# Optimization experiments

Measured on AMD Instinct MI355X. Metric: run time of the kernel, lower is better.

## Reference

```python
import jax, jax.numpy as jnp
import numpy as np

NUM_HEADS = 16
FIELD_SIZE = 512
SIGMA = 3.0
EMB = 1024


def _causal_kernel_fft(G, sigma):
    # kernel[i] = exp(-|i - G//2| / sigma) for i < G//2, else 0; normalized
    i = np.arange(G)
    dist = np.abs(i - G // 2)
    kernel = np.where(i >= G // 2, 0.0, np.exp(-dist / sigma)).astype(np.float32)
    kernel = kernel / (kernel.sum() + 1e-8)
    return jnp.asarray(np.fft.rfft(kernel), dtype=jnp.complex64)


def setup_inputs() -> dict:
    key = jax.random.key(0)
    ks = jax.random.split(key, 9)
    B, N, D = 4, 4096, EMB
    s = 1.0 / np.sqrt(D)
    return {
        "x": jax.random.normal(ks[0], (B, N, D), dtype=jnp.float32),
        "q_w": jax.random.uniform(ks[1], (D, D), minval=-s, maxval=s, dtype=jnp.float32),
        "q_b": jnp.zeros((D,), jnp.float32),
        "k_w": jax.random.uniform(ks[2], (D, D), minval=-s, maxval=s, dtype=jnp.float32),
        "k_b": jnp.zeros((D,), jnp.float32),
        "v_w": jax.random.uniform(ks[3], (D, D), minval=-s, maxval=s, dtype=jnp.float32),
        "v_b": jnp.zeros((D,), jnp.float32),
        "out_w": jax.random.uniform(ks[4], (D, D), minval=-s, maxval=s, dtype=jnp.float32),
        "out_b": jnp.zeros((D,), jnp.float32),
    }


def reference(x, q_w, q_b, k_w, k_b, v_w, v_b, out_w, out_b):
    B, N, D = x.shape
    H, hd, G = NUM_HEADS, D // NUM_HEADS, FIELD_SIZE

    # projections (q is computed in the original but unused downstream)
    q = x @ q_w.T + q_b  # noqa: F841 (faithful to original)
    k = (x @ k_w.T + k_b).reshape(B, N, H, hd).transpose(0, 2, 1, 3)  # (B,H,N,hd)
    v = (x @ v_w.T + v_b).reshape(B, N, H, hd).transpose(0, 2, 1, 3)

    # map sequence positions -> field bins (same for all b, h)
    pos = jnp.arange(N, dtype=jnp.float32) / max(N - 1, 1) * (G - 1)
    field_idx = jnp.clip(pos.astype(jnp.int32), 0, G - 1)  # (N,)

    # weighted values by key magnitude
    k_mag = jnp.linalg.norm(k, axis=-1, keepdims=True)  # (B,H,N,1)
    wv = v * k_mag  # (B,H,N,hd)

    # scatter-add tokens into field bins (vectorized over B,H,hd)
    field = jax.ops.segment_sum(wv.transpose(2, 0, 1, 3), field_idx,
                                num_segments=G)  # (G,B,H,hd)
    field = field.transpose(1, 2, 0, 3)  # (B,H,G,hd)

    # causal convolution along the field via FFT (circular, as in original)
    kfft = _causal_kernel_fft(G, SIGMA)
    f_fft = jnp.fft.rfft(field, n=G, axis=2)
    conv = jnp.fft.irfft(f_fft * kfft[None, None, :, None], n=G, axis=2)

    # gather back to token positions
    out = conv[:, :, field_idx, :]  # (B,H,N,hd)
    out = out.transpose(0, 2, 1, 3).reshape(B, N, D)
    return out @ out_w.T + out_b
```

## Files before the change

### kernel.cpp

```cpp
#include <hip/hip_runtime.h>
#include <hip/hip_bf16.h>

#define NPOS 4096
#define DIM  1024
#define GSZ  512

#define GAS __attribute__((address_space(1)))
#define LAS __attribute__((address_space(3)))

typedef __attribute__((ext_vector_type(8))) short bf16x8;
typedef __attribute__((ext_vector_type(4))) float f32x4;

__device__ __forceinline__ void async_load16(const void* g, void* l) {
  __builtin_amdgcn_global_load_lds((const GAS void*)g, (LAS void*)l, 16, 0, 0);
}

__device__ __forceinline__ int fidx_of(int n) {
  return (int)(((float)n / 4095.0f) * 511.0f);
}

__device__ __forceinline__ float bf2f(unsigned short s) {
  union { unsigned u; float f; } v; v.u = ((unsigned)s) << 16; return v.f;
}

__device__ __forceinline__ int bin_start(int g) {
  if (g >= GSZ) return NPOS;
  int i0 = (g * 4095 + 510) / 511;
  while (i0 > 0 && fidx_of(i0 - 1) >= g) --i0;
  while (i0 < NPOS && fidx_of(i0) < g) ++i0;
  return i0;
}

__device__ __forceinline__ void bin_range(int g, int& i0, int& i1) {
  i0 = bin_start(g);
  i1 = bin_start(g + 1);
}

__global__ __launch_bounds__(256) void cast_all(
    const float* __restrict__ x, const float* __restrict__ kw,
    const float* __restrict__ vw, const float* __restrict__ ow,
    __hip_bfloat16* __restrict__ xb, __hip_bfloat16* __restrict__ kvwb,
    __hip_bfloat16* __restrict__ outwb) {
  int blk = blockIdx.x;
  const float* src; __hip_bfloat16* dst; int off;
  if (blk < 8192)      { src = x;  dst = xb;              off = blk; }
  else if (blk < 8704) { src = kw; dst = kvwb;            off = blk - 8192; }
  else if (blk < 9216) { src = vw; dst = kvwb + 1048576;  off = blk - 8704; }
  else                 { src = ow; dst = outwb;           off = blk - 9216; }
  int i = (off * 256 + threadIdx.x) * 8;
  float4 f0 = *(const float4*)(src + i);
  float4 f1 = *(const float4*)(src + i + 4);
  ushort4 o0, o1;
  __hip_bfloat16 t;
  t = __float2bfloat16(f0.x); o0.x = *(unsigned short*)&t;
  t = __float2bfloat16(f0.y); o0.y = *(unsigned short*)&t;
  t = __float2bfloat16(f0.z); o0.z = *(unsigned short*)&t;
  t = __float2bfloat16(f0.w); o0.w = *(unsigned short*)&t;
  t = __float2bfloat16(f1.x); o1.x = *(unsigned short*)&t;
  t = __float2bfloat16(f1.y); o1.y = *(unsigned short*)&t;
  t = __float2bfloat16(f1.z); o1.z = *(unsigned short*)&t;
  t = __float2bfloat16(f1.w); o1.w = *(unsigned short*)&t;
  *(ushort4*)(dst + i) = o0;
  *(ushort4*)(dst + i + 4) = o1;
}


#define BAR()   __builtin_amdgcn_s_barrier()
#define LGKM0() do { asm volatile("s_waitcnt lgkmcnt(0)" ::: "memory"); \
                     __builtin_amdgcn_sched_barrier(0); } while (0)
#define VMW(N)  asm volatile("s_waitcnt vmcnt(" #N ")" ::: "memory")

#define STAGE_A(BUF, KT, C) \
  async_load16(ag0 + (size_t)(KT) * 64 + (size_t)(C) * 65536, &As[BUF][(C) * 4096 + ldst])
#define STAGE_B(BUF, KT, C) \
  async_load16(bg0 + (size_t)(KT) * 64 + (size_t)(C) * 65536, &Bs[BUF][(C) * 4096 + ldst])

#define STAGE_FULL(BUF, KT) do { \
    _Pragma("unroll") \
    for (int c_ = 0; c_ < 4; ++c_) { \
      STAGE_A(BUF, KT, c_); \
      STAGE_B(BUF, KT, c_); \
    } \
  } while (0)

#define LDA(BUF, MT, CB) (*(const bf16x8*)&As[BUF][abase + (MT) * 1024 + (CB)])
#define LDB(BUF, NT, CB) (*(const bf16x8*)&Bs[BUF][bbase + (NT) * 1024 + (CB)])

#define MFMA_Q(MQ, NQ, BF) do { \
    __builtin_amdgcn_s_setprio(1); \
    _Pragma("unroll") \
    for (int m_ = 0; m_ < 4; ++m_) { \
      _Pragma("unroll") \
      for (int n_ = 0; n_ < 2; ++n_) { \
        acc[(MQ)*4+m_][(NQ)*2+n_] = __builtin_amdgcn_mfma_f32_16x16x32_bf16( \
            af[m_][0], BF[n_][0], acc[(MQ)*4+m_][(NQ)*2+n_], 0, 0, 0); \
        acc[(MQ)*4+m_][(NQ)*2+n_] = __builtin_amdgcn_mfma_f32_16x16x32_bf16( \
            af[m_][1], BF[n_][1], acc[(MQ)*4+m_][(NQ)*2+n_], 0, 0, 0); \
      } \
    } \
    __builtin_amdgcn_s_setprio(0); \
  } while (0)

#define DO_TILE(BUF, KT) do { \
    const bool pf_ = (KT) + 2 < 16; \
     \
    _Pragma("unroll") \
    for (int m_ = 0; m_ < 4; ++m_) { af[m_][0] = LDA(BUF, m_, cb0); af[m_][1] = LDA(BUF, m_, cb1); } \
    _Pragma("unroll") \
    for (int n_ = 0; n_ < 2; ++n_) { b0f[n_][0] = LDB(BUF, n_, cb0); b0f[n_][1] = LDB(BUF, n_, cb1); } \
    BAR(); LGKM0(); \
    MFMA_Q(0, 0, b0f); \
    BAR(); \
     \
    _Pragma("unroll") \
    for (int n_ = 0; n_ < 2; ++n_) { b1f[n_][0] = LDB(BUF, 2 + n_, cb0); b1f[n_][1] = LDB(BUF, 2 + n_, cb1); } \
    if (pf_) { STAGE_A(BUF, (KT) + 2, 0); STAGE_A(BUF, (KT) + 2, 2); } \
    BAR(); LGKM0(); \
    MFMA_Q(0, 1, b1f); \
    BAR(); \
     \
    _Pragma("unroll") \
    for (int m_ = 0; m_ < 4; ++m_) { af[m_][0] = LDA(BUF, 4 + m_, cb0); af[m_][1] = LDA(BUF, 4 + m_, cb1); } \
    if (pf_) { STAGE_B(BUF, (KT) + 2, 0); STAGE_B(BUF, (KT) + 2, 1); \
               STAGE_B(BUF, (KT) + 2, 2); STAGE_B(BUF, (KT) + 2, 3); } \
    BAR(); LGKM0(); \
    MFMA_Q(1, 1, b1f); \
    BAR(); \
     \
    if (pf_) { STAGE_A(BUF, (KT) + 2, 1); STAGE_A(BUF, (KT) + 2, 3); } \
    MFMA_Q(1, 0, b0f); \
    if (pf_) { VMW(8); } else if ((KT) == 14) { VMW(0); } \
    BAR(); \
  } while (0)

__global__ __launch_bounds__(512, 2) void gemm_kv(
    const __hip_bfloat16* __restrict__ A,
    const __hip_bfloat16* __restrict__ B,
    const float* __restrict__ k_b, const float* __restrict__ v_b,
    __hip_bfloat16* __restrict__ Vb, float* __restrict__ knorm) {
  __shared__ __align__(16) __hip_bfloat16 As[2][16384];
  __shared__ __align__(16) __hip_bfloat16 Bs[2][16384];
  const int tid = threadIdx.x;

  const int l   = blockIdx.y * 64 + blockIdx.x;
  const int xcd = l & 7, j = l >> 3;
  const int bx  = xcd * 8 + (j & 7), by = j >> 3;
  const int bm  = bx * 256;

  const int sb  = ((((tid & 7) * 16) ^ (((tid >> 3) & 7) << 4)) >> 1);
  const int r0  = tid >> 3;
  const __hip_bfloat16* ag0 = A + (size_t)(bm + r0) * 1024 + sb;
  const __hip_bfloat16* bg0 = B + (size_t)(by * 256 + r0) * 1024 + sb;
  const int ldst = tid * 8;

  const int wave = tid >> 6, lane = tid & 63;
  const int wr = wave >> 2, wc = wave & 3;
  const int m16 = lane & 15, quad = lane >> 4;
  const int swz  = (m16 & 7) << 4;
  const int cb0  = ((quad * 16)      ^ swz) >> 1;
  const int cb1  = ((quad * 16 + 64) ^ swz) >> 1;
  const int abase = wr * 8192 + m16 * 64;
  const int bbase = wc * 4096 + m16 * 64;

  f32x4 acc[8][4];
#pragma unroll
  for (int i = 0; i < 8; i++)
#pragma unroll
    for (int j2 = 0; j2 < 4; j2++) acc[i][j2] = (f32x4)0.f;

  bf16x8 af[4][2], b0f[2][2], b1f[2][2];

  STAGE_FULL(0, 0);
  STAGE_FULL(1, 1);
  VMW(8);
  BAR();

  for (int kt = 0; kt < 16; kt += 2) {
    DO_TILE(0, kt);
    DO_TILE(1, kt + 1);
  }

  if (by < 4) {
    const int head = by * 4 + wc;
    float bv[4];
#pragma unroll
    for (int nt = 0; nt < 4; nt++) bv[nt] = k_b[by * 256 + wc * 64 + nt * 16 + m16];
#pragma unroll
    for (int mt = 0; mt < 8; mt++) {
#pragma unroll
      for (int r = 0; r < 4; r++) {
        float s = 0.f;
#pragma unroll
        for (int nt = 0; nt < 4; nt++) {
          float t = acc[mt][nt][r] + bv[nt];
          s += t * t;
        }
        s += __shfl_xor(s, 1);
        s += __shfl_xor(s, 2);
        s += __shfl_xor(s, 4);
        s += __shfl_xor(s, 8);
        if (m16 == 0) {
          int row = bm + wr * 128 + mt * 16 + quad * 4 + r;
          knorm[(size_t)row * 16 + head] = sqrtf(s);
        }
      }
    }
  } else {
    const int colb = (by - 4) * 256 + wc * 64;
#pragma unroll
    for (int mt = 0; mt < 8; mt++) {
#pragma unroll
      for (int nt = 0; nt < 4; nt++) {
        int col = colb + nt * 16 + m16;
        float bvv = v_b[col];
#pragma unroll
        for (int r = 0; r < 4; r++) {
          int row = bm + wr * 128 + mt * 16 + quad * 4 + r;
          Vb[(size_t)row * 1024 + col] = __float2bfloat16(acc[mt][nt][r] + bvv);
        }
      }
    }
  }
}

__global__ __launch_bounds__(256) void gemm_outc(
    const __hip_bfloat16* __restrict__ A,
    const __hip_bfloat16* __restrict__ B,
    const float* __restrict__ bias,
    float* __restrict__ C) {
  const int K = 1024;
  __shared__ __align__(16) __hip_bfloat16 Aso[64 * 32];
  __shared__ __align__(16) __hip_bfloat16 Bso[64 * 32];
  __shared__ __align__(16) float ctile[64 * 68];
  const int tid = threadIdx.x;
  const int bm = blockIdx.x * 64, bn = blockIdx.y * 64;

  const int srow = tid >> 2;
  const int scol = (tid & 3) * 8;
  const __hip_bfloat16* ap = A + (size_t)(bm + srow) * K + scol;
  const __hip_bfloat16* bp = B + (size_t)(bn + srow) * K + scol;
  __hip_bfloat16* as = &Aso[srow * 32 + scol];
  __hip_bfloat16* bs = &Bso[srow * 32 + scol];

  const int wave = tid >> 6, lane = tid & 63;
  const int wm = (wave >> 1) * 32, wn = (wave & 1) * 32;
  const int m16 = lane & 15, quad = lane >> 4;

  f32x4 acc[2][2];
#pragma unroll
  for (int i = 0; i < 2; i++)
#pragma unroll
    for (int j = 0; j < 2; j++) acc[i][j] = (f32x4)0.f;

  for (int k0 = 0; k0 < K; k0 += 32) {
    async_load16(ap + k0, as);
    async_load16(bp + k0, bs);
    __syncthreads();
    bf16x8 afr[2], bfr[2];
#pragma unroll
    for (int mt = 0; mt < 2; mt++)
      afr[mt] = *(const bf16x8*)&Aso[(wm + mt * 16 + m16) * 32 + quad * 8];
#pragma unroll
    for (int nt = 0; nt < 2; nt++)
      bfr[nt] = *(const bf16x8*)&Bso[(wn + nt * 16 + m16) * 32 + quad * 8];
#pragma unroll
    for (int mt = 0; mt < 2; mt++)
#pragma unroll
      for (int nt = 0; nt < 2; nt++)
        acc[mt][nt] = __builtin_amdgcn_mfma_f32_16x16x32_bf16(afr[mt], bfr[nt], acc[mt][nt], 0, 0, 0);
    __syncthreads();
  }

#pragma unroll
  for (int mt = 0; mt < 2; mt++) {
#pragma unroll
    for (int nt = 0; nt < 2; nt++) {
      int lcol = wn + nt * 16 + m16;
      float bv = bias[bn + lcol];
#pragma unroll
      for (int r = 0; r < 4; r++) {
        int lrow = wm + mt * 16 + quad * 4 + r;
        ctile[lrow * 68 + lcol] = acc[mt][nt][r] + bv;
      }
    }
  }
  __syncthreads();

  const int b  = bm >> 9;
  const int g0 = bm & (GSZ - 1);
  const int n0 = bin_start(g0);
  const int n1 = bin_start(g0 + 64);
  const int total = (n1 - n0) * 16;
  float* obase = C + (((size_t)b << 12)) * DIM + bn;
  for (int idx = tid; idx < total; idx += 256) {
    int n  = n0 + (idx >> 4);
    int c4 = (idx & 15) * 4;
    int lg = fidx_of(n) - g0;
    float4 v = *(const float4*)&ctile[lg * 68 + c4];
    *(float4*)(obase + (size_t)n * DIM + c4) = v;
  }
}

__global__ __launch_bounds__(256) void wv_field_kernel(
    const __hip_bfloat16* __restrict__ V, const float* __restrict__ knorm,
    float* __restrict__ field) {
  const int b = blockIdx.x, g = blockIdx.y;
  int i0, i1;
  bin_range(g, i0, i1);
  int cnt = i1 - i0;
  if (cnt > 9) cnt = 9;
  __shared__ float km[9][16];
  const int tid = threadIdx.x;
  if (tid < 144) {
    int r = tid >> 4, h = tid & 15;
    km[r][h] = (r < cnt) ? knorm[(size_t)(b * NPOS + i0 + r) * 16 + h] : 0.f;
  }
  __syncthreads();
  const int c0 = tid * 4, h = tid >> 4;
  const unsigned short* vbase = (const unsigned short*)V + (size_t)(b * NPOS + i0) * 1024 + c0;
  ushort4 vv[8];
  float ww[8];
#pragma unroll
  for (int j = 0; j < 8; ++j) {
    int jc = (j < cnt) ? j : 0;
    vv[j] = *(const ushort4*)(vbase + (size_t)jc * 1024);
    ww[j] = (j < cnt) ? km[j][h] : 0.f;
  }
  float a0 = 0.f, a1 = 0.f, a2 = 0.f, a3 = 0.f;
#pragma unroll
  for (int j = 0; j < 8; ++j) {
    a0 += ww[j] * bf2f(vv[j].x); a1 += ww[j] * bf2f(vv[j].y);
    a2 += ww[j] * bf2f(vv[j].z); a3 += ww[j] * bf2f(vv[j].w);
  }
  if (cnt == 9) {
    ushort4 v8 = *(const ushort4*)(vbase + (size_t)8 * 1024);
    float w8 = km[8][h];
    a0 += w8 * bf2f(v8.x); a1 += w8 * bf2f(v8.y);
    a2 += w8 * bf2f(v8.z); a3 += w8 * bf2f(v8.w);
  }
  *(float4*)(field + ((size_t)(b * GSZ + g)) * DIM + c0) = make_float4(a0, a1, a2, a3);
}

__global__ __launch_bounds__(256) void conv_ema_kernel(
    const float* __restrict__ field, __hip_bfloat16* __restrict__ convb) {
  const int b = blockIdx.x, h = blockIdx.y, n0 = blockIdx.z * 64;
  __shared__ float slab[128 * 64];
  const int tid = threadIdx.x;
  const float* fb = field + (size_t)b * GSZ * DIM + h * 64;
  for (int i = tid; i < 128 * 16; i += 256) {
    int row = i >> 4, c4 = i & 15;
    int gg = (n0 + 257 + row) & (GSZ - 1);
    *(float4*)&slab[row * 64 + c4 * 4] = *(const float4*)(fb + (size_t)gg * DIM + c4 * 4);
  }
  __syncthreads();
  const float a = 0.71653131057378927f;
  const float w1 = 1.0f - a;
  const int c = tid & 63, sub = tid >> 6;
  const int e0 = sub * 16;
  float acc = 0.f;
#pragma unroll 4
  for (int t = e0 + 79; t >= e0 + 16; --t)
    acc = w1 * slab[t * 64 + c] + a * acc;
#pragma unroll
  for (int t = e0 + 15; t >= e0; --t) {
    acc = w1 * slab[t * 64 + c] + a * acc;
    convb[((size_t)(b * GSZ) + n0 + t) * DIM + h * 64 + c] = __float2bfloat16(acc);
  }
}

extern "C" void kernel_launch(void* const* d_in, const int* in_sizes, int n_in,
                              void* d_out, int out_size, void* d_ws, size_t ws_size,
                              hipStream_t stream) {
  (void)in_sizes; (void)n_in; (void)out_size; (void)ws_size;
  const float* x     = (const float*)d_in[0];
  const float* k_w   = (const float*)d_in[3];
  const float* k_b   = (const float*)d_in[4];
  const float* v_w   = (const float*)d_in[5];
  const float* v_b   = (const float*)d_in[6];
  const float* out_w = (const float*)d_in[7];
  const float* out_b = (const float*)d_in[8];

  char* p = (char*)d_ws;
  __hip_bfloat16* xb    = (__hip_bfloat16*)p;         p += (size_t)16384 * 1024 * 2;
  __hip_bfloat16* kvwb  = (__hip_bfloat16*)p; p += (size_t)2048 * 1024 * 2;
  __hip_bfloat16* outwb = (__hip_bfloat16*)p; p += (size_t)1024 * 1024 * 2;
  __hip_bfloat16* Vb    = (__hip_bfloat16*)p; p += (size_t)16384 * 1024 * 2;
  float*          knorm = (float*)p;          p += (size_t)16384 * 16 * 4;
  float*          field = (float*)p;          p += (size_t)4 * 512 * 1024 * 4;
  __hip_bfloat16* convb = (__hip_bfloat16*)p;

  cast_all<<<9728, 256, 0, stream>>>(x, k_w, v_w, out_w, xb, kvwb, outwb);

  gemm_kv<<<dim3(64, 8), 512, 0, stream>>>(xb, kvwb, k_b, v_b, Vb, knorm);

  wv_field_kernel<<<dim3(4, 512), 256, 0, stream>>>(Vb, knorm, field);
  conv_ema_kernel<<<dim3(4, 16, 8), 256, 0, stream>>>(field, convb);

  gemm_outc<<<dim3(32, 16), 256, 0, stream>>>(convb, outwb, out_b, (float*)d_out);
}
```

Before: 243.7 us.

## Enlarge output GEMM tiles to 128x128 and remap KV GEMM block order

The output GEMM moves from 64x64 to 128x128 tiles with a K step of 64 split into two 32-wide LDS halves, giving each wave a 4x4 MFMA accumulator grid and fewer barriers per K. The scatter epilogue and ctile are resized to match. The grid shrinks from 512 to 128 blocks, which cuts operand reloads but may leave many CUs idle on a 256-CU part. The KV GEMM block-to-tile mapping is also changed to a different XCD-aware ordering for cache locality.

```diff
diff --git a/kernel.cpp b/kernel.cpp
--- a/kernel.cpp
+++ b/kernel.cpp
@@ -142,10 +142,10 @@
   __shared__ __align__(16) __hip_bfloat16 Bs[2][16384];
   const int tid = threadIdx.x;
 
-  const int l   = blockIdx.y * 64 + blockIdx.x;
-  const int xcd = l & 7, j = l >> 3;
-  const int bx  = xcd * 8 + (j & 7), by = j >> 3;
-  const int bm  = bx * 256;
+  const int l  = blockIdx.y * 64 + blockIdx.x;
+  const int vv = (l & 7) * 64 + (l >> 3);
+  const int bx = vv & 63, by = vv >> 6;
+  const int bm = bx * 256;
 
   const int sb  = ((((tid & 7) * 16) ^ (((tid >> 3) & 7) << 4)) >> 1);
   const int r0  = tid >> 3;
@@ -229,58 +229,68 @@
     const float* __restrict__ bias,
     float* __restrict__ C) {
   const int K = 1024;
-  __shared__ __align__(16) __hip_bfloat16 Aso[64 * 32];
-  __shared__ __align__(16) __hip_bfloat16 Bso[64 * 32];
-  __shared__ __align__(16) float ctile[64 * 68];
+  __shared__ __align__(16) __hip_bfloat16 Aso[2][128 * 32];
+  __shared__ __align__(16) __hip_bfloat16 Bso[2][128 * 32];
+  __shared__ __align__(16) float ctile[128 * 132];
   const int tid = threadIdx.x;
-  const int bm = blockIdx.x * 64, bn = blockIdx.y * 64;
+  const int bm = blockIdx.x * 128, bn = blockIdx.y * 128;
 
   const int srow = tid >> 2;
   const int scol = (tid & 3) * 8;
-  const __hip_bfloat16* ap = A + (size_t)(bm + srow) * K + scol;
-  const __hip_bfloat16* bp = B + (size_t)(bn + srow) * K + scol;
-  __hip_bfloat16* as = &Aso[srow * 32 + scol];
-  __hip_bfloat16* bs = &Bso[srow * 32 + scol];
+  const __hip_bfloat16* ap0 = A + (size_t)(bm + srow) * K + scol;
+  const __hip_bfloat16* ap1 = A + (size_t)(bm + srow + 64) * K + scol;
+  const __hip_bfloat16* bp0 = B + (size_t)(bn + srow) * K + scol;
+  const __hip_bfloat16* bp1 = B + (size_t)(bn + srow + 64) * K + scol;
+  const int soff = srow * 32 + scol;
 
   const int wave = tid >> 6, lane = tid & 63;
-  const int wm = (wave >> 1) * 32, wn = (wave & 1) * 32;
+  const int wm = (wave >> 1) * 64, wn = (wave & 1) * 64;
   const int m16 = lane & 15, quad = lane >> 4;
 
-  f32x4 acc[2][2];
-#pragma unroll
-  for (int i = 0; i < 2; i++)
-#pragma unroll
-    for (int j = 0; j < 2; j++) acc[i][j] = (f32x4)0.f;
-
-  for (int k0 = 0; k0 < K; k0 += 32) {
-    async_load16(ap + k0, as);
-    async_load16(bp + k0, bs);
+  f32x4 acc[4][4];
+#pragma unroll
+  for (int i = 0; i < 4; i++)
+#pragma unroll
+    for (int j = 0; j < 4; j++) acc[i][j] = (f32x4)0.f;
+
+  for (int k0 = 0; k0 < K; k0 += 64) {
+    async_load16(ap0 + k0, &Aso[0][soff]);
+    async_load16(ap1 + k0, &Aso[0][soff + 64 * 32]);
+    async_load16(bp0 + k0, &Bso[0][soff]);
+    async_load16(bp1 + k0, &Bso[0][soff + 64 * 32]);
+    async_load16(ap0 + k0 + 32, &Aso[1][soff]);
+    async_load16(ap1 + k0 + 32, &Aso[1][soff + 64 * 32]);
+    async_load16(bp0 + k0 + 32, &Bso[1][soff]);
+    async_load16(bp1 + k0 + 32, &Bso[1][soff + 64 * 32]);
     __syncthreads();
-    bf16x8 afr[2], bfr[2];
-#pragma unroll
-    for (int mt = 0; mt < 2; mt++)
-      afr[mt] = *(const bf16x8*)&Aso[(wm + mt * 16 + m16) * 32 + quad * 8];
-#pragma unroll
-    for (int nt = 0; nt < 2; nt++)
-      bfr[nt] = *(const bf16x8*)&Bso[(wn + nt * 16 + m16) * 32 + quad * 8];
-#pragma unroll
-    for (int mt = 0; mt < 2; mt++)
-#pragma unroll
-      for (int nt = 0; nt < 2; nt++)
-        acc[mt][nt] = __builtin_amdgcn_mfma_f32_16x16x32_bf16(afr[mt], bfr[nt], acc[mt][nt], 0, 0, 0);
+#pragma unroll
+    for (int h = 0; h < 2; h++) {
+      bf16x8 af[4], bfr[4];
+#pragma unroll
+      for (int mt = 0; mt < 4; mt++)
+        af[mt] = *(const bf16x8*)&Aso[h][(wm + mt * 16 + m16) * 32 + quad * 8];
+#pragma unroll
+      for (int nt = 0; nt < 4; nt++)
+        bfr[nt] = *(const bf16x8*)&Bso[h][(wn + nt * 16 + m16) * 32 + quad * 8];
+#pragma unroll
+      for (int mt = 0; mt < 4; mt++)
+#pragma unroll
+        for (int nt = 0; nt < 4; nt++)
+          acc[mt][nt] = __builtin_amdgcn_mfma_f32_16x16x32_bf16(af[mt], bfr[nt], acc[mt][nt], 0, 0, 0);
+    }
     __syncthreads();
   }
 
 #pragma unroll
-  for (int mt = 0; mt < 2; mt++) {
-#pragma unroll
-    for (int nt = 0; nt < 2; nt++) {
+  for (int mt = 0; mt < 4; mt++) {
+#pragma unroll
+    for (int nt = 0; nt < 4; nt++) {
       int lcol = wn + nt * 16 + m16;
       float bv = bias[bn + lcol];
 #pragma unroll
       for (int r = 0; r < 4; r++) {
         int lrow = wm + mt * 16 + quad * 4 + r;
-        ctile[lrow * 68 + lcol] = acc[mt][nt][r] + bv;
+        ctile[lrow * 132 + lcol] = acc[mt][nt][r] + bv;
       }
     }
   }
@@ -289,14 +299,14 @@
   const int b  = bm >> 9;
   const int g0 = bm & (GSZ - 1);
   const int n0 = bin_start(g0);
-  const int n1 = bin_start(g0 + 64);
-  const int total = (n1 - n0) * 16;
+  const int n1 = bin_start(g0 + 128);
+  const int total = (n1 - n0) * 32;
   float* obase = C + (((size_t)b << 12)) * DIM + bn;
   for (int idx = tid; idx < total; idx += 256) {
-    int n  = n0 + (idx >> 4);
-    int c4 = (idx & 15) * 4;
+    int n  = n0 + (idx >> 5);
+    int c4 = (idx & 31) * 4;
     int lg = fidx_of(n) - g0;
-    float4 v = *(const float4*)&ctile[lg * 68 + c4];
+    float4 v = *(const float4*)&ctile[lg * 132 + c4];
     *(float4*)(obase + (size_t)n * DIM + c4) = v;
   }
 }
@@ -396,5 +406,5 @@
   wv_field_kernel<<<dim3(4, 512), 256, 0, stream>>>(Vb, knorm, field);
   conv_ema_kernel<<<dim3(4, 16, 8), 256, 0, stream>>>(field, convb);
 
-  gemm_outc<<<dim3(32, 16), 256, 0, stream>>>(convb, outwb, out_b, (float*)d_out);
-}
+  gemm_outc<<<dim3(16, 8), 256, 0, stream>>>(convb, outwb, out_b, (float*)d_out);
+}
```

New measurement: 253.5 us. 1.04x slower.
